# Kernel tuning notes

Measured on AMD Instinct MI355X. Metric: run time of the kernel, lower is better.

Reference implementation:

```python
import jax, jax.numpy as jnp
import numpy as np

D_BINS = 16   # piecewise-linear bins
N_PROP = 10   # hard-coded in CountModule.__init__


def pwl(w, x):
    """PiecewiseLinear.forward: w is [D_BINS+1], x any shape in [0,1]."""
    aw = jnp.abs(w)
    nw = aw / aw.sum()
    cs = jnp.cumsum(nw)               # [17] cumulative knot values
    xd = x * D_BINS
    ip = jnp.floor(xd).astype(jnp.int32)   # x >= 0 so trunc == floor
    frac = xd - ip.astype(x.dtype)
    return cs[jnp.minimum(ip, D_BINS)] + frac * nw[jnp.minimum(ip + 1, D_BINS)]


def iou(a):
    """Pairwise IoU of boxes a [B,4,n] (coords y1,x1,y2,x2) -> [B,n,n]."""
    tl = jnp.maximum(a[:, :2, :, None], a[:, :2, None, :])  # [B,2,n,n]
    br = jnp.minimum(a[:, 2:, :, None], a[:, 2:, None, :])
    wh = jnp.clip(br - tl, 0.0)
    inter = wh[:, 0] * wh[:, 1]                               # [B,n,n]
    area = jnp.clip(a[:, 2] - a[:, 0], 0.0) * jnp.clip(a[:, 3] - a[:, 1], 0.0)  # [B,n]
    return inter / (area[:, :, None] + area[:, None, :] - inter + 1e-12)


def count_forward(boxes, attention, f_weights):
    n = N_PROP
    B = boxes.shape[0]
    f = lambda i, x: pwl(f_weights[i], x)
    # keep top-n proposals by attention score
    att_v, idx = jax.lax.top_k(attention, n)                  # [B,n]
    boxes_f = jnp.take_along_axis(
        boxes, jnp.broadcast_to(idx[:, None, :], (B, 4, n)), axis=2)  # [B,4,n]
    att = jax.nn.sigmoid(att_v)
    A = att[:, :, None] * att[:, None, :]                     # outer product [B,n,n]
    Dm = 1.0 - iou(boxes_f)                                   # [B,n,n]
    A_t = f(0, A) * f(1, Dm)
    X = f(3, A) * f(4, Dm)
    # deduplicate: outer_diff on 2D att gives pairwise |a_i - a_j|; on 3D X the
    # original torch code unsqueezes both operands at the same axis, yielding zeros
    att_diff = jnp.abs(att[:, :, None] - att[:, None, :])     # [B,n,n]
    xs = X[:, :, None, :]
    score_diff = jnp.broadcast_to(jnp.abs(xs - xs), (B, n, n, n))  # zeros, as in torch
    sim = f(2, 1.0 - att_diff) * jnp.prod(f(2, 1.0 - score_diff), axis=1)  # [B,n,n]
    s_i = sim.sum(axis=2)                                     # [B,n]
    s_st = s_i[:, :, None] * s_i[:, None, :]                  # [B,n,n]
    score = A_t / s_st
    corr = f(0, att * att) / s_i
    mod_E = score.sum(axis=(1, 2))[:, None] + corr.sum(axis=1, keepdims=True)  # [B,1]
    c = jnp.sqrt(mod_E + 1e-20)
    # to_k_hot: soft two-hot over counts 0..n
    cc = jnp.clip(c, 0.0, float(n))                           # [B,1]
    ip = jnp.floor(cc).astype(jnp.int32)
    frac = cc - ip.astype(cc.dtype)
    left = jax.nn.one_hot(jnp.minimum(ip[:, 0], n), n + 1, dtype=cc.dtype)
    right = jax.nn.one_hot(jnp.minimum(ip[:, 0] + 1, n), n + 1, dtype=cc.dtype)
    o = (1.0 - frac) * left + frac * right                    # [B,n+1]
    p_a = jnp.abs(f(5, att) - 0.5)                            # [B,n]
    p_d = jnp.abs(f(6, Dm) - 0.5)                             # [B,n,n]
    gate = f(7, p_a.mean(axis=1, keepdims=True)
             + p_d.mean(axis=2).mean(axis=1, keepdims=True))  # [B,1]
    return gate * o                                           # [B,n+1]


def setup_inputs() -> dict:
    key = jax.random.key(0)
    k1, k2, k3 = jax.random.split(key, 3)
    B, M = 32768, 36
    boxes = jax.random.uniform(k1, (B, 4, M), dtype=jnp.float32)
    attention = jax.random.normal(k2, (B, M), dtype=jnp.float32)
    f_weights = jax.random.uniform(k3, (8, D_BINS + 1), dtype=jnp.float32,
                                   minval=0.25, maxval=1.75)
    return {"boxes": boxes, "attention": attention, "f_weights": f_weights}


def reference(boxes, attention, f_weights):
    return count_forward(boxes, attention, f_weights)
```

## Files before the change

kernel.cpp:

```cpp
#include <hip/hip_runtime.h>
#include <cstdint>
#include <cstddef>

#define MM 36
#define NP 10
#define BLOCK 256
#define GPB (BLOCK / 16)

template<int CTRL>
__device__ __forceinline__ float dpp_movf(float x) {
    return __int_as_float(__builtin_amdgcn_update_dpp(
        0, __float_as_int(x), CTRL, 0xF, 0xF, true));
}
__device__ __forceinline__ float rowmax16(float x) {
    x = fmaxf(x, dpp_movf<0xB1>(x));
    x = fmaxf(x, dpp_movf<0x4E>(x));
    x = fmaxf(x, dpp_movf<0x141>(x));
    x = fmaxf(x, dpp_movf<0x140>(x));
    return x;
}
__device__ __forceinline__ float rowsum16(float x) {
    x += dpp_movf<0xB1>(x);
    x += dpp_movf<0x4E>(x);
    x += dpp_movf<0x141>(x);
    x += dpp_movf<0x140>(x);
    return x;
}

__device__ __forceinline__ float pwl_eval(const float2* __restrict__ Trow, float x) {
    float xd = x * 16.0f;
    float fip = floorf(xd);
    float frac = xd - fip;
    int ip = (int)fip;
    ip = ip < 0 ? 0 : (ip > 16 ? 16 : ip);
    float2 t = Trow[ip];
    return t.x + frac * t.y;
}

__global__ __launch_bounds__(BLOCK) void count_kernel(
    const float* __restrict__ boxes,
    const float* __restrict__ attention,
    const float* __restrict__ fw,
    float* __restrict__ out,
    int B)
{
    __shared__ float2 T[8][17];
    __shared__ float2 prop[GPB][NP][3];
    __shared__ __align__(8) float invl[GPB][NP];

    const int tid = threadIdx.x;

    if (tid < 8) {
        const float* w = fw + tid * 17;
        float aw[17];
        float s = 0.f;
        #pragma unroll
        for (int k = 0; k < 17; ++k) { aw[k] = fabsf(w[k]); s += aw[k]; }
        float nw[17];
        #pragma unroll
        for (int k = 0; k < 17; ++k) nw[k] = aw[k] / s;
        float c = 0.f;
        #pragma unroll
        for (int k = 0; k < 17; ++k) {
            c += nw[k];
            T[tid][k] = make_float2(c, (k < 16) ? nw[k + 1] : nw[16]);
        }
    }

    const int lane = tid & 63;
    const int l    = tid & 15;
    const int g    = tid >> 4;
    int b = blockIdx.x * GPB + g;
    const bool valid = (b < B);
    b = valid ? b : (B - 1);

    const float* arow = attention + (size_t)b * MM;
    const float* brow = boxes + (size_t)b * (4 * MM);

    float v0 = arow[l];
    float v1 = arow[l + 16];
    float v2 = (l < 4) ? arow[l + 32] : -INFINITY;

    __syncthreads();

    unsigned long long packed = 0ull;
    const int gbase = lane & 48;
    #pragma unroll
    for (int t = 0; t < NP; ++t) {
        float vm = rowmax16(fmaxf(fmaxf(v0, v1), v2));
        unsigned long long b0 = __ballot(v0 == vm);
        unsigned long long b1 = __ballot(v1 == vm);
        unsigned long long b2 = __ballot(v2 == vm);
        unsigned g0 = (unsigned)((b0 >> gbase) & 0xFFFFull);
        unsigned g1 = (unsigned)((b1 >> gbase) & 0xFFFFull);
        unsigned g2 = (unsigned)((b2 >> gbase) & 0xFFFFull);
        int m = g0 ? (__ffs(g0) - 1)
              : (g1 ? (__ffs(g1) + 15)
                    : (__ffs(g2) + 31));
        packed |= ((unsigned long long)m) << (6 * t);
        v0 = (m == l)      ? -INFINITY : v0;
        v1 = (m == l + 16) ? -INFINITY : v1;
        v2 = (m == l + 32) ? -INFINITY : v2;
    }

    float sattI = 0.f, y1I = 0.f, x1I = 0.f, y2I = 0.f, x2I = 0.f, areaI = 0.f;
    if (l < NP) {
        int mo = (int)((packed >> (6 * l)) & 63ull);
        float av = arow[mo];
        sattI = 1.0f / (1.0f + __expf(-av));
        y1I = brow[mo];
        x1I = brow[mo + MM];
        y2I = brow[mo + 2 * MM];
        x2I = brow[mo + 3 * MM];
        areaI = fmaxf(y2I - y1I, 0.f) * fmaxf(x2I - x1I, 0.f);
        prop[g][l][0] = make_float2(y1I, x1I);
        prop[g][l][1] = make_float2(y2I, x2I);
        prop[g][l][2] = make_float2(areaI, sattI);
    }

    float cs2_16 = T[2][16].x;
    float p2 = cs2_16 * cs2_16;
    float p4 = p2 * p2;
    float p8 = p4 * p4;
    float P = p8 * p2;

    const float2* T0 = &T[0][0];
    const float2* T1 = &T[1][0];
    const float2* T2 = &T[2][0];
    const float2* T5 = &T[5][0];
    const float2* T6 = &T[6][0];
    const float2* T7 = &T[7][0];

    float at[NP];
    float s_i = 0.f, pdAcc = 0.f;
    #pragma unroll
    for (int j = 0; j < NP; ++j) {
        float2 p0 = prop[g][j][0];
        float2 p1 = prop[g][j][1];
        float2 p2v = prop[g][j][2];
        float ty = fmaxf(y1I, p0.x);
        float tx = fmaxf(x1I, p0.y);
        float by = fminf(y2I, p1.x);
        float bx = fminf(x2I, p1.y);
        float inter = fmaxf(by - ty, 0.f) * fmaxf(bx - tx, 0.f);
        float iouv = __fdividef(inter, areaI + p2v.x - inter + 1e-12f);
        float Dm = fmaxf(1.0f - iouv, 0.0f);
        float A = sattI * p2v.y;
        at[j] = pwl_eval(T0, A) * pwl_eval(T1, Dm);
        s_i += pwl_eval(T2, 1.0f - fabsf(sattI - p2v.y)) * P;
        pdAcc += fabsf(pwl_eval(T6, Dm) - 0.5f);
    }

    float inv_i = 1.0f / s_i;
    if (l < NP) invl[g][l] = inv_i;

    float dot = 0.f;
    const float2* ivp = reinterpret_cast<const float2*>(&invl[g][0]);
    #pragma unroll
    for (int jj = 0; jj < NP / 2; ++jj) {
        float2 iv = ivp[jj];
        dot = fmaf(at[2 * jj], iv.x, dot);
        dot = fmaf(at[2 * jj + 1], iv.y, dot);
    }

    float corr = pwl_eval(T0, sattI * sattI) * inv_i;
    float fmask = (l < NP) ? 1.f : 0.f;
    float contrib = fmask * (inv_i * dot + corr);
    float pav = fmask * fabsf(pwl_eval(T5, sattI) - 0.5f);
    float pdv = fmask * pdAcc;

    contrib = rowsum16(contrib);
    pav = rowsum16(pav);
    pdv = rowsum16(pdv);

    float gate = pwl_eval(T7, pav * 0.1f + pdv * 0.01f);
    float cval = sqrtf(contrib + 1e-20f);
    cval = fminf(fmaxf(cval, 0.f), 10.0f);
    float fip = floorf(cval);
    int ipc = (int)fip;
    float frac = cval - fip;
    int i0 = ipc < 10 ? ipc : 10;
    int i1 = (ipc + 1) < 10 ? (ipc + 1) : 10;

    if (valid && l < NP + 1) {
        float val = ((l == i0) ? (1.0f - frac) * gate : 0.f)
                  + ((l == i1) ? frac * gate : 0.f);
        out[(size_t)b * (NP + 1) + l] = val;
    }
}

extern "C" void kernel_launch(void* const* d_in, const int* in_sizes, int n_in,
                              void* d_out, int out_size, void* d_ws, size_t ws_size,
                              hipStream_t stream) {
    const float* boxes = (const float*)d_in[0];
    const float* attention = (const float*)d_in[1];
    const float* fw = (const float*)d_in[2];
    float* out = (float*)d_out;
    int B = in_sizes[1] / MM;
    int grid = (B + GPB - 1) / GPB;
    hipLaunchKernelGGL(count_kernel, dim3(grid), dim3(BLOCK), 0, stream,
                       boxes, attention, fw, out, B);
}
```

Before: 24.64 us.

## Stage box rows in LDS with vector loads and merge pwl tables

Box rows are now loaded with coalesced float4 reads before the barrier and staged in shared memory. The per-proposal gather then reads from LDS instead of doing dependent global loads after top-k. The top-k value is carried in a register rather than re-read from global memory. The two lookup tables indexed by Dm are interleaved into one float4 table so a single LDS read serves both, and the proposal data is packed into float4/float2. The cost is more shared memory per block and loading every box value even though only ten per row are used.

After: 23.69 us. 1.04x faster.

```diff
diff --git a/kernel.cpp b/kernel.cpp
--- a/kernel.cpp
+++ b/kernel.cpp
@@ -27,14 +27,13 @@
     return x;
 }
 
-__device__ __forceinline__ float pwl_eval(const float2* __restrict__ Trow, float x) {
+__device__ __forceinline__ float pwl2(const float2* __restrict__ Trow, float x) {
     float xd = x * 16.0f;
     float fip = floorf(xd);
     float frac = xd - fip;
-    int ip = (int)fip;
-    ip = ip < 0 ? 0 : (ip > 16 ? 16 : ip);
+    int ip = (int)fminf(fip, 16.0f);
     float2 t = Trow[ip];
-    return t.x + frac * t.y;
+    return fmaf(frac, t.y, t.x);
 }
 
 __global__ __launch_bounds__(BLOCK) void count_kernel(
@@ -45,10 +44,31 @@
     int B)
 {
     __shared__ float2 T[8][17];
-    __shared__ float2 prop[GPB][NP][3];
+    __shared__ float4 T16[17];
+    __shared__ float  boxrow[GPB][4 * MM];
+    __shared__ float4 propA[GPB][NP];
+    __shared__ float2 propB[GPB][NP];
     __shared__ __align__(8) float invl[GPB][NP];
 
     const int tid = threadIdx.x;
+    const int lane = tid & 63;
+    const int l    = tid & 15;
+    const int g    = tid >> 4;
+    int b = blockIdx.x * GPB + g;
+    const bool valid = (b < B);
+    b = valid ? b : (B - 1);
+
+    const float* arow = attention + (size_t)b * MM;
+    const float4* brow4 = reinterpret_cast<const float4*>(boxes + (size_t)b * (4 * MM));
+
+    float v0 = arow[l];
+    float v1 = arow[l + 16];
+    float v2 = -INFINITY;
+    if (l < 4) v2 = arow[l + 32];
+    float4 B0 = brow4[l];
+    float4 B1 = brow4[l + 16];
+    float4 B2 = make_float4(0.f, 0.f, 0.f, 0.f);
+    if (l < 4) B2 = brow4[l + 32];
 
     if (tid < 8) {
         const float* w = fw + tid * 17;
@@ -66,38 +86,34 @@
             T[tid][k] = make_float2(c, (k < 16) ? nw[k + 1] : nw[16]);
         }
     }
-
-    const int lane = tid & 63;
-    const int l    = tid & 15;
-    const int g    = tid >> 4;
-    int b = blockIdx.x * GPB + g;
-    const bool valid = (b < B);
-    b = valid ? b : (B - 1);
-
-    const float* arow = attention + (size_t)b * MM;
-    const float* brow = boxes + (size_t)b * (4 * MM);
-
-    float v0 = arow[l];
-    float v1 = arow[l + 16];
-    float v2 = (l < 4) ? arow[l + 32] : -INFINITY;
+    if (tid < 17) {
+        float2 a = T[1][tid];
+        float2 c = T[6][tid];
+        T16[tid] = make_float4(a.x, a.y, c.x, c.y);
+    }
+
+    float4* bls = reinterpret_cast<float4*>(&boxrow[g][0]);
+    bls[l] = B0;
+    bls[l + 16] = B1;
+    if (l < 4) bls[l + 32] = B2;
 
     __syncthreads();
 
-    unsigned long long packed = 0ull;
-    const int gbase = lane & 48;
+    const int gbase = tid & 48;
+    int mi = 0; float mv = 0.f;
     #pragma unroll
     for (int t = 0; t < NP; ++t) {
         float vm = rowmax16(fmaxf(fmaxf(v0, v1), v2));
         unsigned long long b0 = __ballot(v0 == vm);
         unsigned long long b1 = __ballot(v1 == vm);
         unsigned long long b2 = __ballot(v2 == vm);
-        unsigned g0 = (unsigned)((b0 >> gbase) & 0xFFFFull);
-        unsigned g1 = (unsigned)((b1 >> gbase) & 0xFFFFull);
-        unsigned g2 = (unsigned)((b2 >> gbase) & 0xFFFFull);
+        unsigned g0 = (unsigned)(b0 >> gbase) & 0xFFFFu;
+        unsigned g1 = (unsigned)(b1 >> gbase) & 0xFFFFu;
+        unsigned g2 = (unsigned)(b2 >> gbase) & 0xFFFFu;
         int m = g0 ? (__ffs(g0) - 1)
               : (g1 ? (__ffs(g1) + 15)
                     : (__ffs(g2) + 31));
-        packed |= ((unsigned long long)m) << (6 * t);
+        if (l == t) { mi = m; mv = vm; }
         v0 = (m == l)      ? -INFINITY : v0;
         v1 = (m == l + 16) ? -INFINITY : v1;
         v2 = (m == l + 32) ? -INFINITY : v2;
@@ -105,17 +121,14 @@
 
     float sattI = 0.f, y1I = 0.f, x1I = 0.f, y2I = 0.f, x2I = 0.f, areaI = 0.f;
     if (l < NP) {
-        int mo = (int)((packed >> (6 * l)) & 63ull);
-        float av = arow[mo];
-        sattI = 1.0f / (1.0f + __expf(-av));
-        y1I = brow[mo];
-        x1I = brow[mo + MM];
-        y2I = brow[mo + 2 * MM];
-        x2I = brow[mo + 3 * MM];
+        sattI = 1.0f / (1.0f + __expf(-mv));
+        y1I = boxrow[g][mi];
+        x1I = boxrow[g][mi + MM];
+        y2I = boxrow[g][mi + 2 * MM];
+        x2I = boxrow[g][mi + 3 * MM];
         areaI = fmaxf(y2I - y1I, 0.f) * fmaxf(x2I - x1I, 0.f);
-        prop[g][l][0] = make_float2(y1I, x1I);
-        prop[g][l][1] = make_float2(y2I, x2I);
-        prop[g][l][2] = make_float2(areaI, sattI);
+        propA[g][l] = make_float4(y1I, x1I, y2I, x2I);
+        propB[g][l] = make_float2(areaI, sattI);
     }
 
     float cs2_16 = T[2][16].x;
@@ -125,30 +138,34 @@
     float P = p8 * p2;
 
     const float2* T0 = &T[0][0];
-    const float2* T1 = &T[1][0];
     const float2* T2 = &T[2][0];
     const float2* T5 = &T[5][0];
-    const float2* T6 = &T[6][0];
     const float2* T7 = &T[7][0];
 
     float at[NP];
     float s_i = 0.f, pdAcc = 0.f;
     #pragma unroll
     for (int j = 0; j < NP; ++j) {
-        float2 p0 = prop[g][j][0];
-        float2 p1 = prop[g][j][1];
-        float2 p2v = prop[g][j][2];
-        float ty = fmaxf(y1I, p0.x);
-        float tx = fmaxf(x1I, p0.y);
-        float by = fminf(y2I, p1.x);
-        float bx = fminf(x2I, p1.y);
+        float4 pj = propA[g][j];
+        float2 qj = propB[g][j];
+        float ty = fmaxf(y1I, pj.x);
+        float tx = fmaxf(x1I, pj.y);
+        float by = fminf(y2I, pj.z);
+        float bx = fminf(x2I, pj.w);
         float inter = fmaxf(by - ty, 0.f) * fmaxf(bx - tx, 0.f);
-        float iouv = __fdividef(inter, areaI + p2v.x - inter + 1e-12f);
+        float iouv = __fdividef(inter, areaI + qj.x - inter + 1e-12f);
         float Dm = fmaxf(1.0f - iouv, 0.0f);
-        float A = sattI * p2v.y;
-        at[j] = pwl_eval(T0, A) * pwl_eval(T1, Dm);
-        s_i += pwl_eval(T2, 1.0f - fabsf(sattI - p2v.y)) * P;
-        pdAcc += fabsf(pwl_eval(T6, Dm) - 0.5f);
+        float A = sattI * qj.y;
+        float xdD = Dm * 16.0f;
+        float fipD = floorf(xdD);
+        float frD = xdD - fipD;
+        int ipD = (int)fminf(fipD, 16.0f);
+        float4 t16 = T16[ipD];
+        float f1v = fmaf(frD, t16.y, t16.x);
+        float f6v = fabsf(fmaf(frD, t16.w, t16.z) - 0.5f);
+        at[j] = pwl2(T0, A) * f1v;
+        s_i += pwl2(T2, 1.0f - fabsf(sattI - qj.y)) * P;
+        pdAcc += f6v;
     }
 
     float inv_i = 1.0f / s_i;
@@ -163,17 +180,17 @@
         dot = fmaf(at[2 * jj + 1], iv.y, dot);
     }
 
-    float corr = pwl_eval(T0, sattI * sattI) * inv_i;
+    float corr = pwl2(T0, sattI * sattI) * inv_i;
     float fmask = (l < NP) ? 1.f : 0.f;
     float contrib = fmask * (inv_i * dot + corr);
-    float pav = fmask * fabsf(pwl_eval(T5, sattI) - 0.5f);
+    float pav = fmask * fabsf(pwl2(T5, sattI) - 0.5f);
     float pdv = fmask * pdAcc;
 
     contrib = rowsum16(contrib);
     pav = rowsum16(pav);
     pdv = rowsum16(pdv);
 
-    float gate = pwl_eval(T7, pav * 0.1f + pdv * 0.01f);
+    float gate = pwl2(T7, pav * 0.1f + pdv * 0.01f);
     float cval = sqrtf(contrib + 1e-20f);
     cval = fminf(fmaxf(cval, 0.f), 10.0f);
     float fip = floorf(cval);
```
